# Performance work log

Hardware: AMD Instinct MI355X
Metric: run time of the kernel (lower is better)

Reference implementation:

```python
import jax, jax.numpy as jnp
import numpy as np

ALPHA = 5.0
EPS = 1e-12  # avoids inf grad of sqrt at the self-distance (exact 0)


def setup_inputs() -> dict:
    key = jax.random.key(0)
    xyz = jax.random.normal(key, (4, 8192, 3), dtype=jnp.float32)
    return {"xyz": xyz, "nbr_size": 2}


def reference(xyz, nbr_size):
    # Brute-force KNN of xyz against itself (self is included with dist 0,
    # matching pointops.knn(query, ref) when query == ref).
    sq = jnp.sum(xyz * xyz, axis=-1)                      # (B, N)
    # squared pairwise distances: ||a||^2 + ||b||^2 - 2 a.b  -> (B, N, N)
    d2 = sq[:, :, None] + sq[:, None, :] - 2.0 * jnp.einsum(
        'bnd,bmd->bnm', xyz, xyz)
    neg_top, _idx = jax.lax.top_k(-d2, nbr_size)          # (B, N, k) smallest d2
    dist = jnp.sqrt(jnp.maximum(-neg_top, EPS))           # Euclidean distance
    dsum = dist.sum(-1)                                   # (B, N)
    avg_dist = dsum.mean(-1, keepdims=True)               # (B, 1)
    # loss = sum of per-point distance sums exceeding alpha * mean
    loss = jnp.where(dsum > avg_dist * ALPHA, dsum, 0.0).sum()
    return loss
```

## Files before the change

### kernel.cpp

```cpp
#include <hip/hip_runtime.h>

#define BB 4
#define NN 8192
#define BN (BB * NN)
#define ALPHA 5.0f
#define EPSF 1e-12f
#define BLOCK 256
#define QPT 2
#define QB (BLOCK * QPT)
#define BIGF 1e30f

template <int NSEG>
__global__ __launch_bounds__(BLOCK) void knn_kernel(
    const float* __restrict__ xyz, float2* __restrict__ pairs) {
  constexpr int SEG = NN / NSEG;
  constexpr int CHUNKS = NN / QB;
  int bid = blockIdx.x;
  int s = bid % NSEG;
  int rem = bid / NSEG;
  int qchunk = rem % CHUNKS;
  int b = rem / CHUNKS;

  const float* xb = xyz + (size_t)b * NN * 3;

  __shared__ float4 tile[SEG];
  int refBase = s * SEG;
#pragma unroll
  for (int r0 = threadIdx.x; r0 < SEG; r0 += BLOCK) {
    int r = refBase + r0;
    tile[r0] = make_float4(xb[3 * r + 0], xb[3 * r + 1], xb[3 * r + 2], 0.0f);
  }

  float qx[QPT], qy[QPT], qz[QPT], m1[QPT], m2[QPT];
#pragma unroll
  for (int i = 0; i < QPT; i++) {
    int q = qchunk * QB + threadIdx.x + i * BLOCK;
    qx[i] = xb[3 * q + 0];
    qy[i] = xb[3 * q + 1];
    qz[i] = xb[3 * q + 2];
    m1[i] = BIGF;
    m2[i] = BIGF;
  }
  __syncthreads();

#pragma unroll 8
  for (int j = 0; j < SEG; j++) {
    float4 p = tile[j];
#pragma unroll
    for (int i = 0; i < QPT; i++) {
      float dx = qx[i] - p.x;
      float dy = qy[i] - p.y;
      float dz = qz[i] - p.z;
      float d2 = fmaf(dx, dx, fmaf(dy, dy, dz * dz));
      float big = fmaxf(d2, m1[i]);
      m1[i] = fminf(m1[i], d2);
      m2[i] = fminf(m2[i], big);
    }
  }

#pragma unroll
  for (int i = 0; i < QPT; i++) {
    int q = qchunk * QB + threadIdx.x + i * BLOCK;
    pairs[(size_t)s * BN + b * NN + q] = make_float2(m1[i], m2[i]);
  }
}

template <int NSEG>
__global__ __launch_bounds__(BLOCK) void merge_kernel(
    const float2* __restrict__ pairs, float* __restrict__ dsum,
    float* __restrict__ partial) {
  int g = blockIdx.x * BLOCK + threadIdx.x;
  float m1 = BIGF, m2 = BIGF;
#pragma unroll
  for (int s = 0; s < NSEG; s++) {
    float2 p = pairs[(size_t)s * BN + g];
    float big = fmaxf(p.x, m1);
    m1 = fminf(m1, p.x);
    m2 = fminf(m2, big);
    big = fmaxf(p.y, m1);
    m1 = fminf(m1, p.y);
    m2 = fminf(m2, big);
  }
  float ds = sqrtf(fmaxf(m1, EPSF)) + sqrtf(fmaxf(m2, EPSF));
  dsum[g] = ds;

  float v = ds;
#pragma unroll
  for (int off = 32; off > 0; off >>= 1) v += __shfl_down(v, off, 64);
  __shared__ float warp_sums[BLOCK / 64];
  if ((threadIdx.x & 63) == 0) warp_sums[threadIdx.x >> 6] = v;
  __syncthreads();
  if (threadIdx.x == 0) {
    float t = 0.0f;
#pragma unroll
    for (int w = 0; w < BLOCK / 64; w++) t += warp_sums[w];
    partial[blockIdx.x] = t;
  }
}

#define LBLK 1024
#define NPART (BN / BLOCK)
#define PPB (NPART / BB)
__global__ __launch_bounds__(LBLK) void loss_kernel(
    const float* __restrict__ dsum, const float* __restrict__ partial,
    float* __restrict__ out) {
  __shared__ float s_avg[BB];
  if (threadIdx.x < BB) {
    float t = 0.0f;
    for (int i = 0; i < PPB; i++) t += partial[threadIdx.x * PPB + i];
    s_avg[threadIdx.x] = t * (ALPHA / NN);
  }
  __syncthreads();

  float acc = 0.0f;
#pragma unroll
  for (int it = 0; it < BN / LBLK; it++) {
    int g = it * LBLK + threadIdx.x;
    float ds = dsum[g];
    float thr = s_avg[g >> 13];
    acc += (ds > thr) ? ds : 0.0f;
  }
#pragma unroll
  for (int off = 32; off > 0; off >>= 1) acc += __shfl_down(acc, off, 64);
  __shared__ float warp_sums[LBLK / 64];
  if ((threadIdx.x & 63) == 0) warp_sums[threadIdx.x >> 6] = acc;
  __syncthreads();
  if (threadIdx.x == 0) {
    float t = 0.0f;
#pragma unroll
    for (int w = 0; w < LBLK / 64; w++) t += warp_sums[w];
    out[0] = t;
  }
}

extern "C" void kernel_launch(void* const* d_in, const int* in_sizes, int n_in,
                              void* d_out, int out_size, void* d_ws,
                              size_t ws_size, hipStream_t stream) {
  const float* xyz = (const float*)d_in[0];
  float* out = (float*)d_out;

  size_t need16 = (size_t)16 * BN * sizeof(float2) + BN * sizeof(float) +
                  NPART * sizeof(float);
  if (ws_size >= need16) {
    float2* pairs = (float2*)d_ws;
    float* dsum = (float*)(pairs + (size_t)16 * BN);
    float* partial = dsum + BN;
    int grid1 = BB * (NN / QB) * 16;
    knn_kernel<16><<<grid1, BLOCK, 0, stream>>>(xyz, pairs);
    merge_kernel<16><<<BN / BLOCK, BLOCK, 0, stream>>>(pairs, dsum, partial);
    loss_kernel<<<1, LBLK, 0, stream>>>(dsum, partial, out);
  } else {
    float2* pairs = (float2*)d_ws;
    float* dsum = (float*)(pairs + (size_t)8 * BN);
    float* partial = dsum + BN;
    int grid1 = BB * (NN / QB) * 8;
    knn_kernel<8><<<grid1, BLOCK, 0, stream>>>(xyz, pairs);
    merge_kernel<8><<<BN / BLOCK, BLOCK, 0, stream>>>(pairs, dsum, partial);
    loss_kernel<<<1, LBLK, 0, stream>>>(dsum, partial, out);
  }
}
```

Before: 104.4 us.

## Use norm-expansion distances, med3 top-2 update, more segments, vectorized loss

The KNN inner loop now computes squared distance as |q|^2 + |p|^2 - 2q·p, with |p|^2 precomputed in the tile's w slot. The top-2 update uses a single med3 instruction, which lowers the ALU op count per pair. Separately, the segment count rises to 32 when the workspace is large enough, giving more blocks. The launch bounds hint 8 waves per SIMD, and the loss kernel uses float4 loads and a shuffle-based partial reduction. The expanded distance formula can lose precision through cancellation, and the self-distance may come out slightly nonzero or negative, which the EPS clamp handles.

Measured after the change: 99.56 us. -4.6%, faster.

```diff
diff --git a/kernel.cpp b/kernel.cpp
--- a/kernel.cpp
+++ b/kernel.cpp
@@ -11,7 +11,7 @@
 #define BIGF 1e30f
 
 template <int NSEG>
-__global__ __launch_bounds__(BLOCK) void knn_kernel(
+__global__ __launch_bounds__(BLOCK, 8) void knn_kernel(
     const float* __restrict__ xyz, float2* __restrict__ pairs) {
   constexpr int SEG = NN / NSEG;
   constexpr int CHUNKS = NN / QB;
@@ -25,19 +25,21 @@
 
   __shared__ float4 tile[SEG];
   int refBase = s * SEG;
-#pragma unroll
   for (int r0 = threadIdx.x; r0 < SEG; r0 += BLOCK) {
     int r = refBase + r0;
-    tile[r0] = make_float4(xb[3 * r + 0], xb[3 * r + 1], xb[3 * r + 2], 0.0f);
+    float px = xb[3 * r + 0], py = xb[3 * r + 1], pz = xb[3 * r + 2];
+    float pp = fmaf(px, px, fmaf(py, py, pz * pz));
+    tile[r0] = make_float4(px, py, pz, pp);
   }
 
-  float qx[QPT], qy[QPT], qz[QPT], m1[QPT], m2[QPT];
+  float qx[QPT], qy[QPT], qz[QPT], qq[QPT], m1[QPT], m2[QPT];
 #pragma unroll
   for (int i = 0; i < QPT; i++) {
     int q = qchunk * QB + threadIdx.x + i * BLOCK;
     qx[i] = xb[3 * q + 0];
     qy[i] = xb[3 * q + 1];
     qz[i] = xb[3 * q + 2];
+    qq[i] = fmaf(qx[i], qx[i], fmaf(qy[i], qy[i], qz[i] * qz[i]));
     m1[i] = BIGF;
     m2[i] = BIGF;
   }
@@ -48,13 +50,11 @@
     float4 p = tile[j];
 #pragma unroll
     for (int i = 0; i < QPT; i++) {
-      float dx = qx[i] - p.x;
-      float dy = qy[i] - p.y;
-      float dz = qz[i] - p.z;
-      float d2 = fmaf(dx, dx, fmaf(dy, dy, dz * dz));
-      float big = fmaxf(d2, m1[i]);
+      float dot = fmaf(qx[i], p.x, fmaf(qy[i], p.y, qz[i] * p.z));
+      float d2 = fmaf(dot, -2.0f, qq[i] + p.w);
+      float nm2 = __builtin_amdgcn_fmed3f(d2, m1[i], m2[i]);
       m1[i] = fminf(m1[i], d2);
-      m2[i] = fminf(m2[i], big);
+      m2[i] = nm2;
     }
   }
 
@@ -71,15 +71,15 @@
     float* __restrict__ partial) {
   int g = blockIdx.x * BLOCK + threadIdx.x;
   float m1 = BIGF, m2 = BIGF;
-#pragma unroll
+#pragma unroll 8
   for (int s = 0; s < NSEG; s++) {
     float2 p = pairs[(size_t)s * BN + g];
-    float big = fmaxf(p.x, m1);
+    float n2 = __builtin_amdgcn_fmed3f(p.x, m1, m2);
     m1 = fminf(m1, p.x);
-    m2 = fminf(m2, big);
-    big = fmaxf(p.y, m1);
+    m2 = n2;
+    n2 = __builtin_amdgcn_fmed3f(p.y, m1, m2);
     m1 = fminf(m1, p.y);
-    m2 = fminf(m2, big);
+    m2 = n2;
   }
   float ds = sqrtf(fmaxf(m1, EPSF)) + sqrtf(fmaxf(m2, EPSF));
   dsum[g] = ds;
@@ -105,20 +105,25 @@
     const float* __restrict__ dsum, const float* __restrict__ partial,
     float* __restrict__ out) {
   __shared__ float s_avg[BB];
-  if (threadIdx.x < BB) {
-    float t = 0.0f;
-    for (int i = 0; i < PPB; i++) t += partial[threadIdx.x * PPB + i];
-    s_avg[threadIdx.x] = t * (ALPHA / NN);
+  if (threadIdx.x < NPART) {
+    float v = partial[threadIdx.x];
+#pragma unroll
+    for (int off = 16; off > 0; off >>= 1) v += __shfl_down(v, off, 32);
+    if ((threadIdx.x & 31) == 0) s_avg[threadIdx.x >> 5] = v * (ALPHA / NN);
   }
   __syncthreads();
 
+  const float4* d4 = (const float4*)dsum;
   float acc = 0.0f;
 #pragma unroll
-  for (int it = 0; it < BN / LBLK; it++) {
-    int g = it * LBLK + threadIdx.x;
-    float ds = dsum[g];
-    float thr = s_avg[g >> 13];
-    acc += (ds > thr) ? ds : 0.0f;
+  for (int it = 0; it < BN / (LBLK * 4); it++) {
+    int idx = it * LBLK + threadIdx.x;
+    float4 v = d4[idx];
+    float thr = s_avg[idx >> 11];
+    acc += (v.x > thr) ? v.x : 0.0f;
+    acc += (v.y > thr) ? v.y : 0.0f;
+    acc += (v.z > thr) ? v.z : 0.0f;
+    acc += (v.w > thr) ? v.w : 0.0f;
   }
 #pragma unroll
   for (int off = 32; off > 0; off >>= 1) acc += __shfl_down(acc, off, 64);
@@ -133,29 +138,32 @@
   }
 }
 
+template <int NSEG>
+static void run(const float* xyz, float* out, void* d_ws, hipStream_t stream) {
+  float2* pairs = (float2*)d_ws;
+  float* dsum = (float*)(pairs + (size_t)NSEG * BN);
+  float* partial = dsum + BN;
+  int grid1 = BB * (NN / QB) * NSEG;
+  knn_kernel<NSEG><<<grid1, BLOCK, 0, stream>>>(xyz, pairs);
+  merge_kernel<NSEG><<<BN / BLOCK, BLOCK, 0, stream>>>(pairs, dsum, partial);
+  loss_kernel<<<1, LBLK, 0, stream>>>(dsum, partial, out);
+}
+
 extern "C" void kernel_launch(void* const* d_in, const int* in_sizes, int n_in,
                               void* d_out, int out_size, void* d_ws,
                               size_t ws_size, hipStream_t stream) {
   const float* xyz = (const float*)d_in[0];
   float* out = (float*)d_out;
 
-  size_t need16 = (size_t)16 * BN * sizeof(float2) + BN * sizeof(float) +
-                  NPART * sizeof(float);
-  if (ws_size >= need16) {
-    float2* pairs = (float2*)d_ws;
-    float* dsum = (float*)(pairs + (size_t)16 * BN);
-    float* partial = dsum + BN;
-    int grid1 = BB * (NN / QB) * 16;
-    knn_kernel<16><<<grid1, BLOCK, 0, stream>>>(xyz, pairs);
-    merge_kernel<16><<<BN / BLOCK, BLOCK, 0, stream>>>(pairs, dsum, partial);
-    loss_kernel<<<1, LBLK, 0, stream>>>(dsum, partial, out);
+  auto need = [](int nseg) {
+    return (size_t)nseg * BN * sizeof(float2) + BN * sizeof(float) +
+           NPART * sizeof(float);
+  };
+  if (ws_size >= need(32)) {
+    run<32>(xyz, out, d_ws, stream);
+  } else if (ws_size >= need(16)) {
+    run<16>(xyz, out, d_ws, stream);
   } else {
-    float2* pairs = (float2*)d_ws;
-    float* dsum = (float*)(pairs + (size_t)8 * BN);
-    float* partial = dsum + BN;
-    int grid1 = BB * (NN / QB) * 8;
-    knn_kernel<8><<<grid1, BLOCK, 0, stream>>>(xyz, pairs);
-    merge_kernel<8><<<BN / BLOCK, BLOCK, 0, stream>>>(pairs, dsum, partial);
-    loss_kernel<<<1, LBLK, 0, stream>>>(dsum, partial, out);
+    run<8>(xyz, out, d_ws, stream);
   }
 }
```
